# Kernel optimization log

Hardware: AMD Instinct MI355X
Metric: run time of the kernel (lower is better)

## Reference

```python
import jax, jax.numpy as jnp
import numpy as np
import math

EMBED_DIM = 768
NUM_FRAMES = 48
NUM_FREQS = 10
C_IN = 3
FOURIER_DIM = 4 * NUM_FREQS  # include_uv=False
PM_HID = C_IN * 9 * 4        # patch_mlp_ratio=4
OM_HID = EMBED_DIM * 4       # out_mlp_ratio=4
B, N, T, H, W = 4, 8192, 48, 256, 256


def setup_inputs() -> dict:
    key = jax.random.key(0)
    ks = jax.random.split(key, 16)
    uv = jax.random.uniform(ks[0], (B, N, 2), dtype=jnp.float32)
    ts = jax.random.randint(ks[1], (B, N, 3), 0, NUM_FRAMES).astype(jnp.float32)
    query = jnp.concatenate([uv, ts], axis=-1)  # (B,N,5)
    images = jax.random.normal(ks[2], (B, C_IN, T, H, W), dtype=jnp.float32)
    def xavier(k, fan_in, fan_out):
        lim = math.sqrt(6.0 / (fan_in + fan_out))
        return jax.random.uniform(k, (fan_in, fan_out), dtype=jnp.float32, minval=-lim, maxval=lim)
    return {
        "query": query,
        "images": images,
        "uv_w": xavier(ks[3], FOURIER_DIM, EMBED_DIM),
        "uv_b": jnp.zeros((EMBED_DIM,), jnp.float32),
        "t_src_emb": 0.02 * jax.random.normal(ks[4], (NUM_FRAMES, EMBED_DIM), dtype=jnp.float32),
        "t_tgt_emb": 0.02 * jax.random.normal(ks[5], (NUM_FRAMES, EMBED_DIM), dtype=jnp.float32),
        "t_cam_emb": 0.02 * jax.random.normal(ks[6], (NUM_FRAMES, EMBED_DIM), dtype=jnp.float32),
        "pm_w1": xavier(ks[7], C_IN * 9, PM_HID),
        "pm_b1": jnp.zeros((PM_HID,), jnp.float32),
        "pm_w2": xavier(ks[8], PM_HID, EMBED_DIM),
        "pm_b2": jnp.zeros((EMBED_DIM,), jnp.float32),
        "om_w1": xavier(ks[9], EMBED_DIM, OM_HID),
        "om_b1": jnp.zeros((OM_HID,), jnp.float32),
        "om_w2": xavier(ks[10], OM_HID, EMBED_DIM),
        "om_b2": jnp.zeros((EMBED_DIM,), jnp.float32),
    }


def reference(query, images, uv_w, uv_b, t_src_emb, t_tgt_emb, t_cam_emb,
              pm_w1, pm_b1, pm_w2, pm_b2, om_w1, om_b1, om_w2, om_b2):
    # images: (B,C,T,H,W) -> (B,T,C,H,W)
    images = jnp.transpose(images, (0, 2, 1, 3, 4))
    Bq, Nq, _ = query.shape
    _, Tq, C, Hh, Ww = images.shape

    uv = jnp.clip(query[..., 0:2].astype(jnp.float32), 0.0, 1.0)  # (B,N,2)
    t_src = jnp.clip(jnp.round(query[..., 2]).astype(jnp.int32), 0, NUM_FRAMES - 1)
    t_tgt = jnp.clip(jnp.round(query[..., 3]).astype(jnp.int32), 0, NUM_FRAMES - 1)
    t_cam = jnp.clip(jnp.round(query[..., 4]).astype(jnp.int32), 0, NUM_FRAMES - 1)

    # Fourier features of (u,v)
    fb = 2.0 ** jnp.arange(NUM_FREQS, dtype=jnp.float32)  # (F,)
    u = uv[..., 0:1]
    v = uv[..., 1:2]
    up = (2.0 * math.pi) * u * fb  # (B,N,F)
    vp = (2.0 * math.pi) * v * fb
    feat = jnp.concatenate([jnp.sin(up), jnp.cos(up), jnp.sin(vp), jnp.cos(vp)], axis=-1)

    token1 = feat @ uv_w + uv_b              # (B,N,D)
    token2 = t_src_emb[t_src]                # embedding lookups
    token3 = t_tgt_emb[t_tgt]
    token4 = t_cam_emb[t_cam]

    # 3x3 patch gather centered at discrete (u,v) pixel of frame t_src
    x = jnp.round(uv[..., 0] * (Ww - 1)).astype(jnp.int32)  # (B,N)
    y = jnp.round(uv[..., 1] * (Hh - 1)).astype(jnp.int32)
    d = jnp.arange(-1, 2, dtype=jnp.int32)
    x_idx = jnp.clip(x[..., None] + d, 0, Ww - 1)  # (B,N,3)
    y_idx = jnp.clip(y[..., None] + d, 0, Hh - 1)  # (B,N,3)
    b_idx = jnp.arange(Bq)[:, None, None, None, None]
    c_idx = jnp.arange(C)[:, None, None]
    # direct fancy-index gather -> (B,N,C,3,3); avoids materializing (B,N,C,H,W)
    patches = images[b_idx,
                     t_src[:, :, None, None, None],
                     c_idx,
                     y_idx[:, :, None, :, None],
                     x_idx[:, :, None, None, :]]
    patch_flat = patches.reshape(Bq, Nq, C * 9)

    h = jax.nn.gelu(patch_flat @ pm_w1 + pm_b1, approximate=False)
    token5 = h @ pm_w2 + pm_b2

    out = token1 + token2 + token3 + token4 + token5
    out = jax.nn.gelu(out @ om_w1 + om_b1, approximate=False) @ om_w2 + om_b2
    return out
```

## Files before the change

kernel.cpp:

```cpp
#include <hip/hip_runtime.h>

typedef __bf16 bf16x8 __attribute__((ext_vector_type(8)));
typedef float  f32x4  __attribute__((ext_vector_type(4)));

#define GAS(p) ((const __attribute__((address_space(1))) void*)(p))
#define LAS(p) ((__attribute__((address_space(3))) void*)(p))

__device__ __forceinline__ float gelu_exact(float x) {
    return 0.5f * x * (1.f + erff(x * 0.70710678118654752440f));
}

__global__ __launch_bounds__(256) void stage1_kernel(
    const float* __restrict__ query, const float* __restrict__ images,
    const float* __restrict__ pm_w1, const float* __restrict__ pm_b1,
    __bf16* __restrict__ G, int* __restrict__ tbuf)
{
    __shared__ float patch[4][28];
    const int wave = threadIdx.x >> 6, lane = threadIdx.x & 63;
    const int p = blockIdx.x * 4 + wave;
    const float* q = query + (size_t)p * 5;
    float u = fminf(fmaxf(q[0], 0.f), 1.f);
    float v = fminf(fmaxf(q[1], 0.f), 1.f);
    int ts = min(max((int)rintf(q[2]), 0), 47);
    int tt = min(max((int)rintf(q[3]), 0), 47);
    int tc = min(max((int)rintf(q[4]), 0), 47);
    const int b = p >> 13;
    if (lane < 27) {
        int c = lane / 9, rem = lane % 9, dy = rem / 3, dx = rem % 3;
        int x = (int)rintf(u * 255.f), y = (int)rintf(v * 255.f);
        int xx = min(max(x + dx - 1, 0), 255);
        int yy = min(max(y + dy - 1, 0), 255);
        size_t idx = ((size_t)((b * 3 + c) * 48 + ts) << 16) + ((size_t)yy << 8) + (size_t)xx;
        patch[wave][lane] = images[idx];
    }
    if (lane < 40) {
        int i = lane % 10;
        float base = (lane < 20) ? u : v;
        float ph = 6.28318530717958647693f * base * exp2f((float)i);
        float val = ((lane / 10) & 1) ? cosf(ph) : sinf(ph);
        G[(size_t)p * 160 + lane] = (__bf16)val;
    }
    if (lane >= 52) G[(size_t)p * 160 + 96 + lane] = (__bf16)0.f;
    if (lane < 3) tbuf[p * 3 + lane] = (lane == 0) ? ts : (lane == 1) ? tt : tc;
    __syncthreads();
    for (int j = lane; j < 108; j += 64) {
        float acc = pm_b1[j];
        #pragma unroll
        for (int i2 = 0; i2 < 27; i2++)
            acc = fmaf(patch[wave][i2], pm_w1[i2 * 108 + j], acc);
        G[(size_t)p * 160 + 40 + j] = (__bf16)gelu_exact(acc);
    }
}

__global__ __launch_bounds__(256) void transpose_to_bf16(
    const float* __restrict__ src, __bf16* __restrict__ dst, int R, int C)
{
    __shared__ float t[32][33];
    const int c0 = blockIdx.x * 32, r0 = blockIdx.y * 32;
    const int tx = threadIdx.x & 31, ty = threadIdx.x >> 5;
    #pragma unroll
    for (int i = 0; i < 32; i += 8)
        t[ty + i][tx] = src[(size_t)(r0 + ty + i) * C + (c0 + tx)];
    __syncthreads();
    #pragma unroll
    for (int i = 0; i < 32; i += 8)
        dst[(size_t)(c0 + ty + i) * R + (r0 + tx)] = (__bf16)t[tx][ty + i];
}

__global__ __launch_bounds__(256) void build_wcat(
    const float* __restrict__ uv_w, const float* __restrict__ pm_w2, __bf16* __restrict__ Wt)
{
    int idx = blockIdx.x * 256 + threadIdx.x;
    int n = idx / 160, k = idx % 160;
    float v = 0.f;
    if (k < 40) v = uv_w[k * 768 + n];
    else if (k < 148) v = pm_w2[(k - 40) * 768 + n];
    Wt[idx] = (__bf16)v;
}

enum { EPI_X = 0, EPI_GELU = 1, EPI_OUT = 2 };

template <int EPI, typename OutT>
__global__ __launch_bounds__(256) void gemm_bt(
    const __bf16* __restrict__ A, const __bf16* __restrict__ Bt, int K,
    const float* __restrict__ bias, const float* __restrict__ bias2,
    const int* __restrict__ tbuf,
    const float* __restrict__ e0, const float* __restrict__ e1, const float* __restrict__ e2,
    OutT* __restrict__ Cmat, int N)
{
    __shared__ __attribute__((aligned(16))) __bf16 As[128 * 32];
    __shared__ __attribute__((aligned(16))) __bf16 Bs[128 * 32];
    const int tid = threadIdx.x;
    const int wave = tid >> 6, lane = tid & 63;
    const int wr = wave >> 1, wc = wave & 1;
    const int quad = lane >> 4, l15 = lane & 15;
    const long m0 = (long)blockIdx.y * 128;
    const long n0 = (long)blockIdx.x * 128;

    f32x4 acc[4][4];
    #pragma unroll
    for (int i = 0; i < 4; i++)
        #pragma unroll
        for (int j = 0; j < 4; j++)
            #pragma unroll
            for (int r = 0; r < 4; r++)
                acc[i][j][r] = 0.f;

    const int ch0 = wave * 64 + lane;
    const int ch1 = (wave + 4) * 64 + lane;
    const __bf16* A0 = A + (m0 + (ch0 >> 2)) * (long)K + (ch0 & 3) * 8;
    const __bf16* A1 = A + (m0 + (ch1 >> 2)) * (long)K + (ch1 & 3) * 8;
    const __bf16* B0 = Bt + (n0 + (ch0 >> 2)) * (long)K + (ch0 & 3) * 8;
    const __bf16* B1 = Bt + (n0 + (ch1 >> 2)) * (long)K + (ch1 & 3) * 8;
    __bf16* lA0 = As + wave * 512;
    __bf16* lA1 = As + (wave + 4) * 512;
    __bf16* lB0 = Bs + wave * 512;
    __bf16* lB1 = Bs + (wave + 4) * 512;

    for (int kt = 0; kt < K; kt += 32) {
        __builtin_amdgcn_global_load_lds(GAS(A0 + kt), LAS(lA0), 16, 0, 0);
        __builtin_amdgcn_global_load_lds(GAS(A1 + kt), LAS(lA1), 16, 0, 0);
        __builtin_amdgcn_global_load_lds(GAS(B0 + kt), LAS(lB0), 16, 0, 0);
        __builtin_amdgcn_global_load_lds(GAS(B1 + kt), LAS(lB1), 16, 0, 0);
        __syncthreads();
        bf16x8 af[4], bfr[4];
        #pragma unroll
        for (int i = 0; i < 4; i++)
            af[i] = *(const bf16x8*)&As[(wr * 64 + i * 16 + l15) * 32 + quad * 8];
        #pragma unroll
        for (int j = 0; j < 4; j++)
            bfr[j] = *(const bf16x8*)&Bs[(wc * 64 + j * 16 + l15) * 32 + quad * 8];
        #pragma unroll
        for (int i = 0; i < 4; i++)
            #pragma unroll
            for (int j = 0; j < 4; j++)
                acc[i][j] = __builtin_amdgcn_mfma_f32_16x16x32_bf16(af[i], bfr[j], acc[i][j], 0, 0, 0);
        __syncthreads();
    }

    #pragma unroll
    for (int i = 0; i < 4; i++) {
        #pragma unroll
        for (int r = 0; r < 4; r++) {
            long row = m0 + wr * 64 + i * 16 + quad * 4 + r;
            int t0 = 0, t1 = 0, t2 = 0;
            if constexpr (EPI == EPI_X) {
                t0 = tbuf[row * 3 + 0];
                t1 = tbuf[row * 3 + 1];
                t2 = tbuf[row * 3 + 2];
            }
            #pragma unroll
            for (int j = 0; j < 4; j++) {
                long col = n0 + wc * 64 + j * 16 + l15;
                float val = acc[i][j][r];
                if constexpr (EPI == EPI_X) {
                    val += bias[col] + bias2[col];
                    val += e0[t0 * 768 + col] + e1[t1 * 768 + col] + e2[t2 * 768 + col];
                    Cmat[row * (long)N + col] = (OutT)val;
                } else if constexpr (EPI == EPI_GELU) {
                    val += bias[col];
                    Cmat[row * (long)N + col] = (OutT)gelu_exact(val);
                } else {
                    val += bias[col];
                    Cmat[row * (long)N + col] = (OutT)val;
                }
            }
        }
    }
}

static constexpr size_t OFF_G  = 0;
static constexpr size_t OFF_T  = 10485760;
static constexpr size_t OFF_WC = 10878976;
static constexpr size_t OFF_W1 = 11124736;
static constexpr size_t OFF_W2 = 15843328;
static constexpr size_t OFF_X  = 20561920;
static constexpr size_t OFF_H2 = 70893568;

extern "C" void kernel_launch(void* const* d_in, const int* in_sizes, int n_in,
                              void* d_out, int out_size, void* d_ws, size_t ws_size,
                              hipStream_t stream)
{
    const float* query  = (const float*)d_in[0];
    const float* images = (const float*)d_in[1];
    const float* uv_w   = (const float*)d_in[2];
    const float* uv_b   = (const float*)d_in[3];
    const float* e_src  = (const float*)d_in[4];
    const float* e_tgt  = (const float*)d_in[5];
    const float* e_cam  = (const float*)d_in[6];
    const float* pm_w1  = (const float*)d_in[7];
    const float* pm_b1  = (const float*)d_in[8];
    const float* pm_w2  = (const float*)d_in[9];
    const float* pm_b2  = (const float*)d_in[10];
    const float* om_w1  = (const float*)d_in[11];
    const float* om_b1  = (const float*)d_in[12];
    const float* om_w2  = (const float*)d_in[13];
    const float* om_b2  = (const float*)d_in[14];
    float* out = (float*)d_out;
    char* ws = (char*)d_ws;

    __bf16* G    = (__bf16*)(ws + OFF_G);
    int*    tb   = (int*)(ws + OFF_T);
    __bf16* Wcat = (__bf16*)(ws + OFF_WC);
    __bf16* W1t  = (__bf16*)(ws + OFF_W1);
    __bf16* W2t  = (__bf16*)(ws + OFF_W2);
    __bf16* X    = (__bf16*)(ws + OFF_X);
    __bf16* H2   = (__bf16*)(ws + OFF_H2);

    stage1_kernel<<<8192, 256, 0, stream>>>(query, images, pm_w1, pm_b1, G, tb);
    transpose_to_bf16<<<dim3(3072 / 32, 768 / 32), 256, 0, stream>>>(om_w1, W1t, 768, 3072);
    transpose_to_bf16<<<dim3(768 / 32, 3072 / 32), 256, 0, stream>>>(om_w2, W2t, 3072, 768);
    build_wcat<<<480, 256, 0, stream>>>(uv_w, pm_w2, Wcat);

    gemm_bt<EPI_X, __bf16><<<dim3(768 / 128, 32768 / 128), 256, 0, stream>>>(
        G, Wcat, 160, uv_b, pm_b2, tb, e_src, e_tgt, e_cam, X, 768);

    long Mc = 1024;
    for (long cand = 32768; cand >= 1024; cand >>= 1)
        if (OFF_H2 + (size_t)cand * 3072 * 2 <= ws_size) { Mc = cand; break; }

    for (long m = 0; m < 32768; m += Mc) {
        gemm_bt<EPI_GELU, __bf16><<<dim3(3072 / 128, Mc / 128), 256, 0, stream>>>(
            X + m * 768, W1t, 768, om_b1, nullptr, nullptr, nullptr, nullptr, nullptr, H2, 3072);
        gemm_bt<EPI_OUT, float><<<dim3(768 / 128, Mc / 128), 256, 0, stream>>>(
            H2, W2t, 3072, om_b2, nullptr, nullptr, nullptr, nullptr, nullptr, out + m * 768, 768);
    }
}
```

Before: 784.1 us.

## Double GEMM K-tile to 64 with XOR-swizzled LDS and grouped block order

The bf16 MFMA GEMM now stages 64-wide K tiles instead of 32, which halves the number of barrier pairs per K loop. LDS columns are XOR-swizzled so the fragment reads avoid bank conflicts. Blocks are launched on a 1D grid remapped into groups of 8 row tiles, to improve L2 reuse of the B matrix. The first GEMM's K is padded from 160 to 192 so it divides by 64, which adds some wasted MFMA work and a larger workspace layout.

```diff
diff --git a/kernel.cpp b/kernel.cpp
--- a/kernel.cpp
+++ b/kernel.cpp
@@ -38,9 +38,9 @@
         float base = (lane < 20) ? u : v;
         float ph = 6.28318530717958647693f * base * exp2f((float)i);
         float val = ((lane / 10) & 1) ? cosf(ph) : sinf(ph);
-        G[(size_t)p * 160 + lane] = (__bf16)val;
-    }
-    if (lane >= 52) G[(size_t)p * 160 + 96 + lane] = (__bf16)0.f;
+        G[(size_t)p * 192 + lane] = (__bf16)val;
+    }
+    for (int j = 148 + lane; j < 192; j += 64) G[(size_t)p * 192 + j] = (__bf16)0.f;
     if (lane < 3) tbuf[p * 3 + lane] = (lane == 0) ? ts : (lane == 1) ? tt : tc;
     __syncthreads();
     for (int j = lane; j < 108; j += 64) {
@@ -48,7 +48,7 @@
         #pragma unroll
         for (int i2 = 0; i2 < 27; i2++)
             acc = fmaf(patch[wave][i2], pm_w1[i2 * 108 + j], acc);
-        G[(size_t)p * 160 + 40 + j] = (__bf16)gelu_exact(acc);
+        G[(size_t)p * 192 + 40 + j] = (__bf16)gelu_exact(acc);
     }
 }
 
@@ -71,7 +71,7 @@
     const float* __restrict__ uv_w, const float* __restrict__ pm_w2, __bf16* __restrict__ Wt)
 {
     int idx = blockIdx.x * 256 + threadIdx.x;
-    int n = idx / 160, k = idx % 160;
+    int n = idx / 192, k = idx % 192;
     float v = 0.f;
     if (k < 40) v = uv_w[k * 768 + n];
     else if (k < 148) v = pm_w2[(k - 40) * 768 + n];
@@ -88,14 +88,20 @@
     const float* __restrict__ e0, const float* __restrict__ e1, const float* __restrict__ e2,
     OutT* __restrict__ Cmat, int N)
 {
-    __shared__ __attribute__((aligned(16))) __bf16 As[128 * 32];
-    __shared__ __attribute__((aligned(16))) __bf16 Bs[128 * 32];
+    __shared__ __attribute__((aligned(16))) __bf16 As[128 * 64];
+    __shared__ __attribute__((aligned(16))) __bf16 Bs[128 * 64];
     const int tid = threadIdx.x;
     const int wave = tid >> 6, lane = tid & 63;
     const int wr = wave >> 1, wc = wave & 1;
     const int quad = lane >> 4, l15 = lane & 15;
-    const long m0 = (long)blockIdx.y * 128;
-    const long n0 = (long)blockIdx.x * 128;
+    const int sw = l15 & 7;
+
+    const int ntiles = N >> 7;
+    const int per_super = ntiles << 3;
+    const int id = blockIdx.x;
+    const int sup = id / per_super, rem = id - sup * per_super;
+    const long m0 = (long)(sup * 8 + (rem & 7)) << 7;
+    const long n0 = (long)(rem >> 3) << 7;
 
     f32x4 acc[4][4];
     #pragma unroll
@@ -106,35 +112,41 @@
             for (int r = 0; r < 4; r++)
                 acc[i][j][r] = 0.f;
 
-    const int ch0 = wave * 64 + lane;
-    const int ch1 = (wave + 4) * 64 + lane;
-    const __bf16* A0 = A + (m0 + (ch0 >> 2)) * (long)K + (ch0 & 3) * 8;
-    const __bf16* A1 = A + (m0 + (ch1 >> 2)) * (long)K + (ch1 & 3) * 8;
-    const __bf16* B0 = Bt + (n0 + (ch0 >> 2)) * (long)K + (ch0 & 3) * 8;
-    const __bf16* B1 = Bt + (n0 + (ch1 >> 2)) * (long)K + (ch1 & 3) * 8;
-    __bf16* lA0 = As + wave * 512;
-    __bf16* lA1 = As + (wave + 4) * 512;
-    __bf16* lB0 = Bs + wave * 512;
-    __bf16* lB1 = Bs + (wave + 4) * 512;
-
-    for (int kt = 0; kt < K; kt += 32) {
-        __builtin_amdgcn_global_load_lds(GAS(A0 + kt), LAS(lA0), 16, 0, 0);
-        __builtin_amdgcn_global_load_lds(GAS(A1 + kt), LAS(lA1), 16, 0, 0);
-        __builtin_amdgcn_global_load_lds(GAS(B0 + kt), LAS(lB0), 16, 0, 0);
-        __builtin_amdgcn_global_load_lds(GAS(B1 + kt), LAS(lB1), 16, 0, 0);
+    const __bf16* pa[4]; const __bf16* pb[4];
+    __bf16* la[4]; __bf16* lb[4];
+    #pragma unroll
+    for (int t = 0; t < 4; t++) {
+        int c = (t * 4 + wave) * 64 + lane;
+        int row = c >> 3, s = c & 7, g = s ^ (row & 7);
+        pa[t] = A  + (m0 + row) * (long)K + g * 8;
+        pb[t] = Bt + (n0 + row) * (long)K + g * 8;
+        la[t] = As + (t * 4 + wave) * 512;
+        lb[t] = Bs + (t * 4 + wave) * 512;
+    }
+
+    for (int kt = 0; kt < K; kt += 64) {
+        #pragma unroll
+        for (int t = 0; t < 4; t++) {
+            __builtin_amdgcn_global_load_lds(GAS(pa[t] + kt), LAS(la[t]), 16, 0, 0);
+            __builtin_amdgcn_global_load_lds(GAS(pb[t] + kt), LAS(lb[t]), 16, 0, 0);
+        }
         __syncthreads();
-        bf16x8 af[4], bfr[4];
-        #pragma unroll
-        for (int i = 0; i < 4; i++)
-            af[i] = *(const bf16x8*)&As[(wr * 64 + i * 16 + l15) * 32 + quad * 8];
-        #pragma unroll
-        for (int j = 0; j < 4; j++)
-            bfr[j] = *(const bf16x8*)&Bs[(wc * 64 + j * 16 + l15) * 32 + quad * 8];
-        #pragma unroll
-        for (int i = 0; i < 4; i++)
+        #pragma unroll
+        for (int h = 0; h < 2; h++) {
+            const int slot = ((h * 4 + quad) ^ sw) * 8;
+            bf16x8 af[4], bfv[4];
+            #pragma unroll
+            for (int i = 0; i < 4; i++)
+                af[i] = *(const bf16x8*)&As[(wr * 64 + i * 16 + l15) * 64 + slot];
             #pragma unroll
             for (int j = 0; j < 4; j++)
-                acc[i][j] = __builtin_amdgcn_mfma_f32_16x16x32_bf16(af[i], bfr[j], acc[i][j], 0, 0, 0);
+                bfv[j] = *(const bf16x8*)&Bs[(wc * 64 + j * 16 + l15) * 64 + slot];
+            #pragma unroll
+            for (int i = 0; i < 4; i++)
+                #pragma unroll
+                for (int j = 0; j < 4; j++)
+                    acc[i][j] = __builtin_amdgcn_mfma_f32_16x16x32_bf16(af[i], bfv[j], acc[i][j], 0, 0, 0);
+        }
         __syncthreads();
     }
 
@@ -170,12 +182,12 @@
 }
 
 static constexpr size_t OFF_G  = 0;
-static constexpr size_t OFF_T  = 10485760;
-static constexpr size_t OFF_WC = 10878976;
-static constexpr size_t OFF_W1 = 11124736;
-static constexpr size_t OFF_W2 = 15843328;
-static constexpr size_t OFF_X  = 20561920;
-static constexpr size_t OFF_H2 = 70893568;
+static constexpr size_t OFF_T  = 12582912;
+static constexpr size_t OFF_WC = 12976128;
+static constexpr size_t OFF_W1 = 13271040;
+static constexpr size_t OFF_W2 = 17989632;
+static constexpr size_t OFF_X  = 22708224;
+static constexpr size_t OFF_H2 = 73039872;
 
 extern "C" void kernel_launch(void* const* d_in, const int* in_sizes, int n_in,
                               void* d_out, int out_size, void* d_ws, size_t ws_size,
@@ -210,19 +222,19 @@
     stage1_kernel<<<8192, 256, 0, stream>>>(query, images, pm_w1, pm_b1, G, tb);
     transpose_to_bf16<<<dim3(3072 / 32, 768 / 32), 256, 0, stream>>>(om_w1, W1t, 768, 3072);
     transpose_to_bf16<<<dim3(768 / 32, 3072 / 32), 256, 0, stream>>>(om_w2, W2t, 3072, 768);
-    build_wcat<<<480, 256, 0, stream>>>(uv_w, pm_w2, Wcat);
-
-    gemm_bt<EPI_X, __bf16><<<dim3(768 / 128, 32768 / 128), 256, 0, stream>>>(
-        G, Wcat, 160, uv_b, pm_b2, tb, e_src, e_tgt, e_cam, X, 768);
+    build_wcat<<<576, 256, 0, stream>>>(uv_w, pm_w2, Wcat);
+
+    gemm_bt<EPI_X, __bf16><<<256 * 6, 256, 0, stream>>>(
+        G, Wcat, 192, uv_b, pm_b2, tb, e_src, e_tgt, e_cam, X, 768);
 
     long Mc = 1024;
     for (long cand = 32768; cand >= 1024; cand >>= 1)
         if (OFF_H2 + (size_t)cand * 3072 * 2 <= ws_size) { Mc = cand; break; }
 
     for (long m = 0; m < 32768; m += Mc) {
-        gemm_bt<EPI_GELU, __bf16><<<dim3(3072 / 128, Mc / 128), 256, 0, stream>>>(
+        gemm_bt<EPI_GELU, __bf16><<<(Mc / 128) * 24, 256, 0, stream>>>(
             X + m * 768, W1t, 768, om_b1, nullptr, nullptr, nullptr, nullptr, nullptr, H2, 3072);
-        gemm_bt<EPI_OUT, float><<<dim3(768 / 128, Mc / 128), 256, 0, stream>>>(
+        gemm_bt<EPI_OUT, float><<<(Mc / 128) * 6, 256, 0, stream>>>(
             H2, W2t, 3072, om_b2, nullptr, nullptr, nullptr, nullptr, nullptr, out + m * 768, 768);
     }
 }
```

After: 705.5 us. 1.11x faster.
